# Kernel tuning notes

Measured on AMD Instinct MI355X. Metric: run time of the kernel, lower is better.

The kernel has to match this reference:

```python
import jax, jax.numpy as jnp
import numpy as np

B, S, P, D = 128, 64, 32, 256   # batch, seq_len, pad_size, input_size
E, H, L, A, O = 256, 128, 2, 1, 2  # embed, hidden, n_layers, att_dim, output
INITRANGE = 0.1


def setup_inputs() -> dict:
    key = jax.random.key(0)
    ks = jax.random.split(key, 12)
    u = lambda k, shape: jax.random.uniform(k, shape, jnp.float32, -INITRANGE, INITRANGE)
    return {
        "inputs": jax.random.normal(ks[0], (B, S, P, D), jnp.float32),
        "conv_w": u(ks[1], (D,)),          # Conv1d(1,1,kernel=D) weight (output length is 1)
        "conv_b": u(ks[2], (1,)),
        "embed_w": u(ks[3], (E, D)),       # Linear(D,E,bias=False)
        "gru_Wih": u(ks[4], (L, 2, 3 * H, E)),  # [layer, direction, 3H, in] (E == 2H)
        "gru_Whh": u(ks[5], (L, 2, 3 * H, H)),
        "gru_bih": u(ks[6], (L, 2, 3 * H)),
        "gru_bhh": u(ks[7], (L, 2, 3 * H)),
        "att_w1": u(ks[8], (A, 2 * H)),    # Linear(2H, att_dim, bias=False)
        "lin_w": u(ks[9], (O, 2 * H)),
        "lin_b": u(ks[10], (O,)),
        "batch_size": B,
    }


def _gru_layer(x, Wih, Whh, bih, bhh, reverse):
    # x: [B,S,Din]; torch GRU cell semantics.
    xg = jnp.einsum('bsd,gd->sbg', x, Wih) + bih  # precompute input gates [S,B,3H]
    h0 = jnp.zeros((x.shape[0], Whh.shape[1]), x.dtype)

    def step(h, xg_t):
        gh = h @ Whh.T + bhh
        xr, xz, xn = jnp.split(xg_t, 3, axis=-1)
        hr, hz, hn = jnp.split(gh, 3, axis=-1)
        r = jax.nn.sigmoid(xr + hr)
        z = jax.nn.sigmoid(xz + hz)
        n = jnp.tanh(xn + r * hn)
        h_new = (1.0 - z) * n + z * h
        return h_new, h_new

    _, hs = jax.lax.scan(step, h0, xg, reverse=reverse)  # [S,B,H], time-aligned
    return jnp.swapaxes(hs, 0, 1)  # [B,S,H]


def _forward(inputs, conv_w, conv_b, embed_w, gru_Wih, gru_Whh, gru_bih, gru_bhh,
             att_w1, lin_w, lin_b, batch_size):
    # convolutional_layer: conv output length is 1 -> per-event scalar dot product,
    # then bmm gives a weighted sum of events within each visit.
    s = jnp.einsum('bspk,k->bsp', inputs, conv_w) + conv_b[0]      # [B,S,P]
    conv_all = jnp.einsum('bsp,bspk->bsk', s, inputs)               # [B,S,D]
    # embedding_layer: Linear(D,E) + Hardtanh
    x = jnp.clip(conv_all @ embed_w.T, -1.0, 1.0)                   # [B,S,E]
    # bidirectional multi-layer GRU, h0 = zeros (dropout_p = 0 -> identity)
    for l in range(L):
        f = _gru_layer(x, gru_Wih[l, 0], gru_Whh[l, 0], gru_bih[l, 0], gru_bhh[l, 0], False)
        b = _gru_layer(x, gru_Wih[l, 1], gru_Whh[l, 1], gru_bih[l, 1], gru_bhh[l, 1], True)
        x = jnp.concatenate([f, b], axis=-1)                        # [B,S,2H]
    states = x
    # add_attention: per-step Linear(2H, att_dim) + softmax over att_dim (nn.Softmax on [B,A])
    alpha = jax.nn.softmax(jnp.einsum('bsh,ah->bsa', states, att_w1), axis=-1)
    alpha = jnp.swapaxes(alpha, 1, 2)                               # [B,A,S]
    context = jnp.einsum('bas,bsh->bah', alpha, states).reshape(batch_size, -1)  # [B, A*2H]
    out = jax.nn.softmax(context @ lin_w.T + lin_b, axis=-1)        # [B,O]
    return out, states, context, alpha


def reference(inputs, conv_w, conv_b, embed_w, gru_Wih, gru_Whh, gru_bih, gru_bhh,
              att_w1, lin_w, lin_b, batch_size):
    return _forward(inputs, conv_w, conv_b, embed_w, gru_Wih, gru_Whh, gru_bih,
                    gru_bhh, att_w1, lin_w, lin_b, batch_size)
```

## Files before the change

### kernel.cpp

```cpp
#include <hip/hip_runtime.h>


using u16 = unsigned short;
using u32 = unsigned int;

typedef __bf16 bf16x8 __attribute__((ext_vector_type(8)));
typedef float  f32x4  __attribute__((ext_vector_type(4)));

__device__ __forceinline__ float bf2f(u16 u) {
  union { u32 i; float f; } v; v.i = ((u32)u) << 16; return v.f;
}
__device__ __forceinline__ u16 f2bf(float f) {
  union { float f; u32 i; } v; v.f = f;
  u32 i = v.i;
  u32 r = (i + 0x7FFFu + ((i >> 16) & 1u)) >> 16;
  return (u16)r;
}
__device__ __forceinline__ float sigm(float x) { return 1.f / (1.f + __expf(-x)); }
__device__ __forceinline__ float tanh_f(float x) { return 1.f - 2.f / (1.f + __expf(2.f * x)); }

__global__ __launch_bounds__(256) void k_cvt(
    const float* __restrict__ embw, const float* __restrict__ Wih,
    u16* __restrict__ embHi, u16* __restrict__ embLo, u16* __restrict__ wihB) {
  const int i = blockIdx.x * 256 + threadIdx.x;
  if (i < 65536) {
    float v = embw[i];
    u16 h = f2bf(v);
    embHi[i] = h;
    embLo[i] = f2bf(v - bf2f(h));
  }
  wihB[i] = f2bf(Wih[i]);
}

__global__ __launch_bounds__(256) void k_conv(
    const float* __restrict__ inp, const float* __restrict__ cw,
    const float* __restrict__ cb, u16* __restrict__ chi, u16* __restrict__ clo) {
  __shared__ float tile[32 * 256];
  __shared__ float cwf[256];
  __shared__ float s_p[32];
  const int bs  = blockIdx.x;
  const int tid = threadIdx.x;
  const float* src = inp + (size_t)bs * 8192;
#pragma unroll
  for (int i = 0; i < 8; i++) {
    int idx = i * 1024 + tid * 4;
    *(float4*)&tile[idx] = *(const float4*)&src[idx];
  }
  cwf[tid] = cw[tid];
  __syncthreads();
  const int wv = tid >> 6, ln = tid & 63;
  const float cbf = cb[0];
  for (int pp = 0; pp < 8; pp++) {
    int p = wv * 8 + pp;
    float part = 0.f;
#pragma unroll
    for (int q = 0; q < 4; q++) {
      int k = ln + q * 64;
      part += tile[p * 256 + k] * cwf[k];
    }
    for (int off = 32; off; off >>= 1) part += __shfl_xor(part, off, 64);
    if (ln == 0) s_p[p] = part + cbf;
  }
  __syncthreads();
  float acc = 0.f;
  const int k = tid;
#pragma unroll
  for (int p = 0; p < 32; p++) acc += s_p[p] * tile[p * 256 + k];
  u16 hi = f2bf(acc);
  float lo = acc - bf2f(hi);
  chi[(size_t)bs * 256 + k] = hi;
  clo[(size_t)bs * 256 + k] = f2bf(lo);
}

template <bool HAS_ALO, bool HAS_WLO, bool HAS_BIAS, bool CLIP, bool OUT_BF16>
__global__ __launch_bounds__(256) void k_gemm(
    const u16* __restrict__ A, const u16* __restrict__ Alo,
    const u16* __restrict__ W, const u16* __restrict__ Wlo,
    const float* __restrict__ bias,
    void* __restrict__ Cout, int M, int N, int K) {
  const int LDT = 56;
  __shared__ u16 As[64 * 56];
  __shared__ u16 La[64 * 56];
  __shared__ u16 Ws[64 * 56];
  __shared__ u16 Lw[64 * 56];
  const int tid = threadIdx.x;
  const int m0 = blockIdx.x * 64, n0 = blockIdx.y * 64;
  const int wv = tid >> 6, ln = tid & 63;
  const int lm = ln & 15, lk = (ln >> 4) * 8;
  const int srow = tid >> 2, sgrp = tid & 3;

  f32x4 acc[4];
#pragma unroll
  for (int nt = 0; nt < 4; nt++) acc[nt] = (f32x4){0.f, 0.f, 0.f, 0.f};

  for (int kc = 0; kc < K; kc += 32) {
    __syncthreads();
    *(uint4*)&As[srow * LDT + sgrp * 8] =
        *(const uint4*)&A[(size_t)(m0 + srow) * K + kc + sgrp * 8];
    *(uint4*)&Ws[srow * LDT + sgrp * 8] =
        *(const uint4*)&W[(size_t)(n0 + srow) * K + kc + sgrp * 8];
    if (HAS_ALO)
      *(uint4*)&La[srow * LDT + sgrp * 8] =
          *(const uint4*)&Alo[(size_t)(m0 + srow) * K + kc + sgrp * 8];
    if (HAS_WLO)
      *(uint4*)&Lw[srow * LDT + sgrp * 8] =
          *(const uint4*)&Wlo[(size_t)(n0 + srow) * K + kc + sgrp * 8];
    __syncthreads();

    bf16x8 af = *(const bf16x8*)&As[(wv * 16 + lm) * LDT + lk];
    bf16x8 bfr[4];
#pragma unroll
    for (int nt = 0; nt < 4; nt++)
      bfr[nt] = *(const bf16x8*)&Ws[(nt * 16 + lm) * LDT + lk];
#pragma unroll
    for (int nt = 0; nt < 4; nt++)
      acc[nt] = __builtin_amdgcn_mfma_f32_16x16x32_bf16(af, bfr[nt], acc[nt], 0, 0, 0);
    if (HAS_ALO) {
      bf16x8 lf = *(const bf16x8*)&La[(wv * 16 + lm) * LDT + lk];
#pragma unroll
      for (int nt = 0; nt < 4; nt++)
        acc[nt] = __builtin_amdgcn_mfma_f32_16x16x32_bf16(lf, bfr[nt], acc[nt], 0, 0, 0);
    }
    if (HAS_WLO) {
#pragma unroll
      for (int nt = 0; nt < 4; nt++) {
        bf16x8 wl = *(const bf16x8*)&Lw[(nt * 16 + lm) * LDT + lk];
        acc[nt] = __builtin_amdgcn_mfma_f32_16x16x32_bf16(af, wl, acc[nt], 0, 0, 0);
      }
    }
  }

  const int rbase = m0 + wv * 16 + (ln >> 4) * 4;
#pragma unroll
  for (int nt = 0; nt < 4; nt++) {
    const int col = n0 + nt * 16 + lm;
    const float bv = HAS_BIAS ? bias[col] : 0.f;
#pragma unroll
    for (int r = 0; r < 4; r++) {
      float v = acc[nt][r] + bv;
      if (CLIP) v = fminf(fmaxf(v, -1.f), 1.f);
      const int row = rbase + r;
      if (OUT_BF16)
        ((u16*)Cout)[(size_t)row * N + col] = f2bf(v);
      else
        ((float*)Cout)[(size_t)row * N + col] = v;
    }
  }
}

__global__ __launch_bounds__(384) void k_gru(
    const float* __restrict__ xg,
    const float* __restrict__ Whh,
    const float* __restrict__ bhh,
    u16* __restrict__ st_bf,
    float* __restrict__ st_f,
    float* __restrict__ ctx) {
  __shared__ float gh[384];
  __shared__ float hf[128];
  const int dir = blockIdx.x & 1, b = blockIdx.x >> 1;
  const int r = threadIdx.x;

  float w[128];
  const float4* wrow = (const float4*)(Whh + ((size_t)dir * 384 + r) * 128);
#pragma unroll
  for (int i = 0; i < 32; i++) {
    float4 q = wrow[i];
    w[4 * i]     = q.x;
    w[4 * i + 1] = q.y;
    w[4 * i + 2] = q.z;
    w[4 * i + 3] = q.w;
  }
  const float bhv = bhh[dir * 384 + r];
  if (r < 128) hf[r] = 0.f;
  float csum = 0.f;
  __syncthreads();

  for (int ti = 0; ti < 64; ti++) {
    const int t = dir ? (63 - ti) : ti;
    float a = bhv;
    const float4* hv = (const float4*)hf;
#pragma unroll
    for (int kk = 0; kk < 32; kk++) {
      float4 h4 = hv[kk];
      a += w[4 * kk] * h4.x + w[4 * kk + 1] * h4.y +
           w[4 * kk + 2] * h4.z + w[4 * kk + 3] * h4.w;
    }
    gh[r] = a;
    __syncthreads();
    if (r < 128) {
      const float* xrow = xg + (size_t)(b * 64 + t) * 768 + dir * 384;
      float xr = xrow[r], xz = xrow[128 + r], xn = xrow[256 + r];
      float rg = sigm(xr + gh[r]);
      float zg = sigm(xz + gh[128 + r]);
      float ng = tanh_f(xn + rg * gh[256 + r]);
      float hp = hf[r];
      float hn = (1.f - zg) * ng + zg * hp;
      hf[r] = hn;
      const size_t oi = (size_t)(b * 64 + t) * 256 + dir * 128 + r;
      if (st_bf) st_bf[oi] = f2bf(hn);
      if (st_f)  st_f[oi]  = hn;
      csum += hn;
    }
    __syncthreads();
  }
  if (ctx != nullptr && r < 128)
    ctx[(size_t)b * 256 + dir * 128 + r] = csum;
}

__global__ __launch_bounds__(256) void k_final(
    const float* __restrict__ ctx, const float* __restrict__ lw,
    const float* __restrict__ lb, float* __restrict__ out,
    float* __restrict__ alpha) {
  const int tid = threadIdx.x;
  if (tid < 128) {
    const int b = tid;
    float a0 = lb[0], a1 = lb[1];
    for (int k = 0; k < 256; k++) {
      float c = ctx[b * 256 + k];
      a0 += c * lw[k];
      a1 += c * lw[256 + k];
    }
    float m = fmaxf(a0, a1);
    float e0 = __expf(a0 - m), e1 = __expf(a1 - m);
    float s = e0 + e1;
    out[2 * b]     = e0 / s;
    out[2 * b + 1] = e1 / s;
  }
  for (int i = tid; i < 8192; i += 256) alpha[i] = 1.0f;
}

extern "C" void kernel_launch(void* const* d_in, const int* in_sizes, int n_in,
                              void* d_out, int out_size, void* d_ws, size_t ws_size,
                              hipStream_t stream) {
  const float* inp   = (const float*)d_in[0];
  const float* convw = (const float*)d_in[1];
  const float* convb = (const float*)d_in[2];
  const float* embw  = (const float*)d_in[3];
  const float* Wih   = (const float*)d_in[4];
  const float* Whh   = (const float*)d_in[5];
  const float* bih   = (const float*)d_in[6];
  const float* bhh   = (const float*)d_in[7];
  const float* lw    = (const float*)d_in[9];
  const float* lb    = (const float*)d_in[10];

  char* ws = (char*)d_ws;
  u16*   convHi = (u16*)(ws);
  u16*   convLo = (u16*)(ws + 4194304u);
  u16*   xbuf   = (u16*)(ws + 8388608u);
  u16*   embHi  = (u16*)(ws + 12582912u);
  u16*   embLo  = (u16*)(ws + 12713984u);
  u16*   wihB   = (u16*)(ws + 12845056u);
  float* xgbuf  = (float*)(ws + 13631488u);
  u16*   states0 = convHi;

  float* outp    = (float*)d_out;
  float* statesO = outp + 256;
  float* ctxO    = outp + 2097408;
  float* alphaO  = outp + 2130176;

  k_cvt<<<1536, 256, 0, stream>>>(embw, Wih, embHi, embLo, wihB);

  k_conv<<<8192, 256, 0, stream>>>(inp, convw, convb, convHi, convLo);

  dim3 gE(128, 4);
  k_gemm<true, true, false, true, true><<<gE, 256, 0, stream>>>(
      convHi, convLo, embHi, embLo, nullptr, xbuf, 8192, 256, 256);

  dim3 gX(128, 12);
  k_gemm<false, false, true, false, false><<<gX, 256, 0, stream>>>(
      xbuf, nullptr, wihB, nullptr, bih, xgbuf, 8192, 768, 256);

  k_gru<<<256, 384, 0, stream>>>(xgbuf, Whh, bhh, states0, nullptr, nullptr);

  k_gemm<false, false, true, false, false><<<gX, 256, 0, stream>>>(
      states0, nullptr, wihB + 196608, nullptr, bih + 768, xgbuf, 8192, 768, 256);

  k_gru<<<256, 384, 0, stream>>>(xgbuf, Whh + 98304, bhh + 768,
                                 nullptr, statesO, ctxO);

  k_final<<<1, 256, 0, stream>>>(ctxO, lw, lb, outp, alphaO);
}
```

Baseline: 612.4 us.

## Compute GRU recurrent matvec with split-bf16 MFMA and double-buffered hidden state

The per-step recurrent h·Whh product moves off scalar FMA loops (one thread per gate row, 128 fp32 weights in registers) and onto MFMA 16x16x32 bf16 instructions. Hidden state and weights are split into hi/lo bf16 pairs so fp32 accuracy is roughly kept, at the cost of three MFMAs per tile. The hidden state is double-buffered in LDS, which drops one barrier per step, and the next step's input-gate values are prefetched into registers. Only 16 of the 64 lanes in each wave do the gate math, and only one of the 16 MFMA rows carries useful data (batch of 1 per block), so most matrix work is wasted.

```diff
diff --git a/kernel.cpp b/kernel.cpp
--- a/kernel.cpp
+++ b/kernel.cpp
@@ -18,6 +18,17 @@
 }
 __device__ __forceinline__ float sigm(float x) { return 1.f / (1.f + __expf(-x)); }
 __device__ __forceinline__ float tanh_f(float x) { return 1.f - 2.f / (1.f + __expf(2.f * x)); }
+
+__device__ __forceinline__ void split8(const float* v, bf16x8& hi, bf16x8& lo) {
+  union { bf16x8 v; u16 s[8]; } H, L;
+#pragma unroll
+  for (int j = 0; j < 8; j++) {
+    u16 h = f2bf(v[j]);
+    H.s[j] = h;
+    L.s[j] = f2bf(v[j] - bf2f(h));
+  }
+  hi = H.v; lo = L.v;
+}
 
 __global__ __launch_bounds__(256) void k_cvt(
     const float* __restrict__ embw, const float* __restrict__ Wih,
@@ -148,63 +159,105 @@
   }
 }
 
-__global__ __launch_bounds__(384) void k_gru(
+__global__ __launch_bounds__(512, 2) void k_gru(
     const float* __restrict__ xg,
-    const float* __restrict__ Whh,
-    const float* __restrict__ bhh,
+    const float* __restrict__ WhhL,
+    const float* __restrict__ bhhL,
     u16* __restrict__ st_bf,
     float* __restrict__ st_f,
     float* __restrict__ ctx) {
-  __shared__ float gh[384];
-  __shared__ float hf[128];
-  const int dir = blockIdx.x & 1, b = blockIdx.x >> 1;
-  const int r = threadIdx.x;
-
-  float w[128];
-  const float4* wrow = (const float4*)(Whh + ((size_t)dir * 384 + r) * 128);
-#pragma unroll
-  for (int i = 0; i < 32; i++) {
-    float4 q = wrow[i];
-    w[4 * i]     = q.x;
-    w[4 * i + 1] = q.y;
-    w[4 * i + 2] = q.z;
-    w[4 * i + 3] = q.w;
-  }
-  const float bhv = bhh[dir * 384 + r];
-  if (r < 128) hf[r] = 0.f;
-  float csum = 0.f;
+  __shared__ __attribute__((aligned(16))) u16 hbHi[2][128];
+  __shared__ __attribute__((aligned(16))) u16 hbLo[2][128];
+
+  const int b   = blockIdx.x >> 1;
+  const int dir = blockIdx.x & 1;
+  const int tid = threadIdx.x;
+  const int w   = tid >> 6, l = tid & 63;
+  const int lm  = l & 15;
+  const int kw  = (l >> 4) * 8;
+  const int d   = w * 16 + lm;
+
+  bf16x8 whi[3][4], wlo[3][4];
+#pragma unroll
+  for (int tt = 0; tt < 3; tt++) {
+#pragma unroll
+    for (int kt = 0; kt < 4; kt++) {
+      const int row = (tt * 8 + w) * 16 + lm;
+      const float* p = WhhL + ((size_t)(dir * 384 + row)) * 128 + kt * 32 + kw;
+      float v[8];
+      *(float4*)&v[0] = *(const float4*)&p[0];
+      *(float4*)&v[4] = *(const float4*)&p[4];
+      split8(v, whi[tt][kt], wlo[tt][kt]);
+    }
+  }
+  float bhr = 0.f, bhz = 0.f, bhn = 0.f;
+  if (l < 16) {
+    bhr = bhhL[dir * 384 + d];
+    bhz = bhhL[dir * 384 + 128 + d];
+    bhn = bhhL[dir * 384 + 256 + d];
+  }
+  if (tid < 128) { hbHi[0][tid] = 0; hbLo[0][tid] = 0; }
+
+  const float* xbase = xg + (size_t)(b * 64) * 768 + dir * 384 + d;
+  float xr = 0.f, xz = 0.f, xn = 0.f;
+  if (l < 16) {
+    const int t0 = dir ? 63 : 0;
+    xr = xbase[t0 * 768];
+    xz = xbase[t0 * 768 + 128];
+    xn = xbase[t0 * 768 + 256];
+  }
+  float hold = 0.f, csum = 0.f;
   __syncthreads();
 
+  int cur = 0;
   for (int ti = 0; ti < 64; ti++) {
     const int t = dir ? (63 - ti) : ti;
-    float a = bhv;
-    const float4* hv = (const float4*)hf;
-#pragma unroll
-    for (int kk = 0; kk < 32; kk++) {
-      float4 h4 = hv[kk];
-      a += w[4 * kk] * h4.x + w[4 * kk + 1] * h4.y +
-           w[4 * kk + 2] * h4.z + w[4 * kk + 3] * h4.w;
-    }
-    gh[r] = a;
+    float nxr = 0.f, nxz = 0.f, nxn = 0.f;
+    if (l < 16 && ti < 63) {
+      const int tn = dir ? (62 - ti) : (ti + 1);
+      nxr = xbase[tn * 768];
+      nxz = xbase[tn * 768 + 128];
+      nxn = xbase[tn * 768 + 256];
+    }
+    bf16x8 ahi[4], alo[4];
+#pragma unroll
+    for (int kt = 0; kt < 4; kt++) {
+      ahi[kt] = *(const bf16x8*)&hbHi[cur][kt * 32 + kw];
+      alo[kt] = *(const bf16x8*)&hbLo[cur][kt * 32 + kw];
+    }
+    f32x4 acc[3];
+#pragma unroll
+    for (int tt = 0; tt < 3; tt++) acc[tt] = (f32x4){0.f, 0.f, 0.f, 0.f};
+#pragma unroll
+    for (int kt = 0; kt < 4; kt++) {
+#pragma unroll
+      for (int tt = 0; tt < 3; tt++) {
+        acc[tt] = __builtin_amdgcn_mfma_f32_16x16x32_bf16(ahi[kt], whi[tt][kt], acc[tt], 0, 0, 0);
+        acc[tt] = __builtin_amdgcn_mfma_f32_16x16x32_bf16(alo[kt], whi[tt][kt], acc[tt], 0, 0, 0);
+        acc[tt] = __builtin_amdgcn_mfma_f32_16x16x32_bf16(ahi[kt], wlo[tt][kt], acc[tt], 0, 0, 0);
+      }
+    }
+    const int nxt = cur ^ 1;
+    if (l < 16) {
+      const float rg = sigm(xr + bhr + acc[0][0]);
+      const float zg = sigm(xz + bhz + acc[1][0]);
+      const float ng = tanh_f(xn + rg * (acc[2][0] + bhn));
+      const float hn = (1.f - zg) * ng + zg * hold;
+      hold = hn;
+      csum += hn;
+      const u16 hh = f2bf(hn);
+      hbHi[nxt][d] = hh;
+      hbLo[nxt][d] = f2bf(hn - bf2f(hh));
+      const size_t oi = (size_t)(b * 64 + t) * 256 + dir * 128 + d;
+      if (st_bf) st_bf[oi] = hh;
+      if (st_f)  st_f[oi]  = hn;
+    }
     __syncthreads();
-    if (r < 128) {
-      const float* xrow = xg + (size_t)(b * 64 + t) * 768 + dir * 384;
-      float xr = xrow[r], xz = xrow[128 + r], xn = xrow[256 + r];
-      float rg = sigm(xr + gh[r]);
-      float zg = sigm(xz + gh[128 + r]);
-      float ng = tanh_f(xn + rg * gh[256 + r]);
-      float hp = hf[r];
-      float hn = (1.f - zg) * ng + zg * hp;
-      hf[r] = hn;
-      const size_t oi = (size_t)(b * 64 + t) * 256 + dir * 128 + r;
-      if (st_bf) st_bf[oi] = f2bf(hn);
-      if (st_f)  st_f[oi]  = hn;
-      csum += hn;
-    }
-    __syncthreads();
-  }
-  if (ctx != nullptr && r < 128)
-    ctx[(size_t)b * 256 + dir * 128 + r] = csum;
+    cur = nxt;
+    xr = nxr; xz = nxz; xn = nxn;
+  }
+  if (ctx != nullptr && l < 16)
+    ctx[(size_t)b * 256 + dir * 128 + d] = csum;
 }
 
 __global__ __launch_bounds__(256) void k_final(
@@ -270,12 +323,12 @@
   k_gemm<false, false, true, false, false><<<gX, 256, 0, stream>>>(
       xbuf, nullptr, wihB, nullptr, bih, xgbuf, 8192, 768, 256);
 
-  k_gru<<<256, 384, 0, stream>>>(xgbuf, Whh, bhh, states0, nullptr, nullptr);
+  k_gru<<<256, 512, 0, stream>>>(xgbuf, Whh, bhh, states0, nullptr, nullptr);
 
   k_gemm<false, false, true, false, false><<<gX, 256, 0, stream>>>(
       states0, nullptr, wihB + 196608, nullptr, bih + 768, xgbuf, 8192, 768, 256);
 
-  k_gru<<<256, 384, 0, stream>>>(xgbuf, Whh + 98304, bhh + 768,
+  k_gru<<<256, 512, 0, stream>>>(xgbuf, Whh + 98304, bhh + 768,
                                  nullptr, statesO, ctxO);
 
   k_final<<<1, 256, 0, stream>>>(ctxO, lw, lb, outp, alphaO);
```

Result: faster. 564.9 us (-7.7%).
